# Performance work log

Hardware: AMD Instinct MI355X
Metric: run time of the kernel (lower is better)

Reference implementation:

```python
import jax, jax.numpy as jnp
import numpy as np

NUM_CLASS = 8192
FEAT_DIM = 512
BATCH = 131072


def setup_inputs() -> dict:
    key = jax.random.key(0)
    k1, k2, k3 = jax.random.split(key, 3)
    batch_samples = jax.random.normal(k1, (BATCH, FEAT_DIM), dtype=jnp.float32)
    class_sums = jnp.zeros((NUM_CLASS, FEAT_DIM), dtype=jnp.float32)
    targets = jax.random.randint(k2, (BATCH,), 0, NUM_CLASS, dtype=jnp.int64)
    idx = jax.random.randint(k3, (BATCH,), 0, BATCH, dtype=jnp.int64)
    return {"batch_samples": batch_samples, "class_sums": class_sums,
            "targets": targets, "idx": idx}


def reference(batch_samples, class_sums, targets, idx):
    # Original forward: for each unique label, class_sums[label] += sum of rows
    # of batch_samples with that label. This is exactly a segment-sum
    # (scatter-add by class label) accumulated into class_sums.
    # idx is unused in the forward math (kept for signature fidelity).
    inc = jax.ops.segment_sum(batch_samples, targets, num_segments=NUM_CLASS)
    return class_sums + inc  # updated class_sums buffer [num_class, feat_dim]
```

## Files before the change

### kernel.cpp

```cpp
#include <hip/hip_runtime.h>
#include <hip/hip_bf16.h>


#define FEAT 512
#define FEAT4 128
#define CAP   128

typedef float f4 __attribute__((ext_vector_type(4)));

__device__ __forceinline__ void bucket_one(int c, int row, int* __restrict__ fill,
                                           int* __restrict__ rows_buf,
                                           int* __restrict__ ovf_cnt,
                                           int* __restrict__ ovf) {
    int pos = atomicAdd(&fill[c], 1);
    if (pos < CAP) rows_buf[c * CAP + pos] = row;
    else           ovf[atomicAdd(ovf_cnt, 1)] = row;
}

__global__ void k_scatter(const int4* __restrict__ t4, int* __restrict__ fill,
                          int* __restrict__ rows_buf, int* __restrict__ ovf_cnt,
                          int* __restrict__ ovf, int n4,
                          const int* __restrict__ targets, int batch) {
    int i = blockIdx.x * blockDim.x + threadIdx.x;
    if (i < n4) {
        int4 v = t4[i];
        int r = i * 4;
        bucket_one(v.x, r + 0, fill, rows_buf, ovf_cnt, ovf);
        bucket_one(v.y, r + 1, fill, rows_buf, ovf_cnt, ovf);
        bucket_one(v.z, r + 2, fill, rows_buf, ovf_cnt, ovf);
        bucket_one(v.w, r + 3, fill, rows_buf, ovf_cnt, ovf);
    }
    if (i == 0) {
        for (int k = n4 * 4; k < batch; ++k)
            bucket_one(targets[k], k, fill, rows_buf, ovf_cnt, ovf);
    }
}

__global__ __launch_bounds__(128) void k_sum(const f4* __restrict__ batch,
                                             const f4* __restrict__ csums,
                                             const int* __restrict__ fill,
                                             const int* __restrict__ rows_buf,
                                             f4* __restrict__ out) {
    const int c = blockIdx.x;
    const int t = threadIdx.x;
    const int n = min(fill[c], CAP);

    __shared__ int sidx[CAP];
    if (t < n) sidx[t] = rows_buf[c * CAP + t];
    __syncthreads();

    f4 acc = csums[(size_t)c * FEAT4 + t];

    int j = 0;
    for (; j + 8 <= n; j += 8) {
        f4 v0 = __builtin_nontemporal_load(&batch[(size_t)sidx[j + 0] * FEAT4 + t]);
        f4 v1 = __builtin_nontemporal_load(&batch[(size_t)sidx[j + 1] * FEAT4 + t]);
        f4 v2 = __builtin_nontemporal_load(&batch[(size_t)sidx[j + 2] * FEAT4 + t]);
        f4 v3 = __builtin_nontemporal_load(&batch[(size_t)sidx[j + 3] * FEAT4 + t]);
        f4 v4 = __builtin_nontemporal_load(&batch[(size_t)sidx[j + 4] * FEAT4 + t]);
        f4 v5 = __builtin_nontemporal_load(&batch[(size_t)sidx[j + 5] * FEAT4 + t]);
        f4 v6 = __builtin_nontemporal_load(&batch[(size_t)sidx[j + 6] * FEAT4 + t]);
        f4 v7 = __builtin_nontemporal_load(&batch[(size_t)sidx[j + 7] * FEAT4 + t]);
        acc += ((v0 + v1) + (v2 + v3)) + ((v4 + v5) + (v6 + v7));
    }
    for (; j < n; ++j)
        acc += __builtin_nontemporal_load(&batch[(size_t)sidx[j] * FEAT4 + t]);

    __builtin_nontemporal_store(acc, &out[(size_t)c * FEAT4 + t]);
}

__global__ __launch_bounds__(128) void k_ovf(const f4* __restrict__ batch,
                                             const int* __restrict__ targets,
                                             const int* __restrict__ ovf_cnt,
                                             const int* __restrict__ ovf,
                                             float* __restrict__ out) {
    const int cnt = *ovf_cnt;
    const int t = threadIdx.x;
    for (int e = blockIdx.x; e < cnt; e += gridDim.x) {
        int row = ovf[e];
        int c = targets[row];
        f4 v = batch[(size_t)row * FEAT4 + t];
        float* o = out + (size_t)c * FEAT + t * 4;
        atomicAdd(o + 0, v.x);
        atomicAdd(o + 1, v.y);
        atomicAdd(o + 2, v.z);
        atomicAdd(o + 3, v.w);
    }
}

__global__ void k_copy(const float4* __restrict__ src, float4* __restrict__ dst, int n4) {
    int i = blockIdx.x * blockDim.x + threadIdx.x;
    if (i < n4) dst[i] = src[i];
}

__global__ __launch_bounds__(128) void k_atomic(const float4* __restrict__ batch,
                                                const int* __restrict__ targets,
                                                float* __restrict__ out, int batch_n) {
    const int r = blockIdx.x;
    const int t = threadIdx.x;
    if (r >= batch_n) return;
    float4 v = batch[(size_t)r * FEAT4 + t];
    float* o = out + (size_t)targets[r] * FEAT + t * 4;
    atomicAdd(o + 0, v.x);
    atomicAdd(o + 1, v.y);
    atomicAdd(o + 2, v.z);
    atomicAdd(o + 3, v.w);
}

extern "C" void kernel_launch(void* const* d_in, const int* in_sizes, int n_in,
                              void* d_out, int out_size, void* d_ws, size_t ws_size,
                              hipStream_t stream) {
    const float* batch_samples = (const float*)d_in[0];
    const float* class_sums    = (const float*)d_in[1];
    const int*   targets       = (const int*)d_in[2];

    const int batch     = in_sizes[2];
    const int num_class = out_size / FEAT;
    float* out = (float*)d_out;

    const size_t rows_off = ((size_t)num_class + 64) & ~63ull;
    const size_t ovf_off  = rows_off + (size_t)num_class * CAP;
    const size_t need     = (ovf_off + (size_t)batch) * 4;

    if (ws_size >= need) {
        int* fill     = (int*)d_ws;
        int* ovf_cnt  = fill + num_class;
        int* rows_buf = fill + rows_off;
        int* ovf      = fill + ovf_off;
        const int n4 = batch / 4;

        (void)hipMemsetAsync(fill, 0, ((size_t)num_class + 1) * 4, stream);
        k_scatter<<<(n4 + 255) / 256, 256, 0, stream>>>((const int4*)targets, fill,
                                                        rows_buf, ovf_cnt, ovf,
                                                        n4, targets, batch);
        k_sum<<<num_class, 128, 0, stream>>>((const f4*)batch_samples,
                                             (const f4*)class_sums,
                                             fill, rows_buf, (f4*)out);
        k_ovf<<<256, 128, 0, stream>>>((const f4*)batch_samples, targets,
                                       ovf_cnt, ovf, out);
    } else {
        const int nv4 = out_size / 4;
        k_copy<<<(nv4 + 255) / 256, 256, 0, stream>>>((const float4*)class_sums,
                                                      (float4*)out, nv4);
        k_atomic<<<batch, 128, 0, stream>>>((const float4*)batch_samples,
                                            targets, out, batch);
    }
}
```

Baseline: 377.2 us.

## Replace bucket-and-gather with column-sliced LDS atomic segment-sum kernel

Drops the three-kernel pipeline (bucket rows by class into a workspace, gather-sum per class, overflow atomics) and uses one kernel of 256 blocks. Each block owns one 16-byte feature column slice and half of the class range. It streams all targets, adds matching rows into a 4x4096 shared-memory accumulator with LDS atomics, then writes the result plus class_sums. This removes the memset, the global bucketing atomics and the index workspace. In exchange every block reads the full targets array, batch reads become strided 16-byte accesses across rows, and shared atomics may contend.

```diff
diff --git a/kernel.cpp b/kernel.cpp
--- a/kernel.cpp
+++ b/kernel.cpp
@@ -1,90 +1,76 @@
 #include <hip/hip_runtime.h>
-#include <hip/hip_bf16.h>
 
 
-#define FEAT 512
-#define FEAT4 128
-#define CAP   128
+#define FEAT   512
+#define FEAT4  128
+#define NCLS_MAX 8192
+#define CSPAN  4096
+#define TPB    1024
 
 typedef float f4 __attribute__((ext_vector_type(4)));
 
-__device__ __forceinline__ void bucket_one(int c, int row, int* __restrict__ fill,
-                                           int* __restrict__ rows_buf,
-                                           int* __restrict__ ovf_cnt,
-                                           int* __restrict__ ovf) {
-    int pos = atomicAdd(&fill[c], 1);
-    if (pos < CAP) rows_buf[c * CAP + pos] = row;
-    else           ovf[atomicAdd(ovf_cnt, 1)] = row;
-}
+__global__ __launch_bounds__(TPB) void k_seg(const f4* __restrict__ batch,
+                                             const f4* __restrict__ csums,
+                                             const int4* __restrict__ t4,
+                                             const int* __restrict__ targets,
+                                             f4* __restrict__ out,
+                                             int batch_n, int num_class) {
+    const int bb = blockIdx.x & 127;
+    const int h  = blockIdx.x >> 7;
+    const int s  = ((bb & 15) << 3) | (bb >> 4);
+    const int cbase = h * CSPAN;
+    const int cspan = min(CSPAN, num_class - cbase);
+    if (cspan <= 0) return;
 
-__global__ void k_scatter(const int4* __restrict__ t4, int* __restrict__ fill,
-                          int* __restrict__ rows_buf, int* __restrict__ ovf_cnt,
-                          int* __restrict__ ovf, int n4,
-                          const int* __restrict__ targets, int batch) {
-    int i = blockIdx.x * blockDim.x + threadIdx.x;
-    if (i < n4) {
-        int4 v = t4[i];
-        int r = i * 4;
-        bucket_one(v.x, r + 0, fill, rows_buf, ovf_cnt, ovf);
-        bucket_one(v.y, r + 1, fill, rows_buf, ovf_cnt, ovf);
-        bucket_one(v.z, r + 2, fill, rows_buf, ovf_cnt, ovf);
-        bucket_one(v.w, r + 3, fill, rows_buf, ovf_cnt, ovf);
-    }
-    if (i == 0) {
-        for (int k = n4 * 4; k < batch; ++k)
-            bucket_one(targets[k], k, fill, rows_buf, ovf_cnt, ovf);
-    }
-}
+    __shared__ float acc[4][CSPAN];
 
-__global__ __launch_bounds__(128) void k_sum(const f4* __restrict__ batch,
-                                             const f4* __restrict__ csums,
-                                             const int* __restrict__ fill,
-                                             const int* __restrict__ rows_buf,
-                                             f4* __restrict__ out) {
-    const int c = blockIdx.x;
-    const int t = threadIdx.x;
-    const int n = min(fill[c], CAP);
-
-    __shared__ int sidx[CAP];
-    if (t < n) sidx[t] = rows_buf[c * CAP + t];
+    f4* accv = (f4*)acc;
+    for (int i = threadIdx.x; i < CSPAN; i += TPB) accv[i] = (f4){0.f, 0.f, 0.f, 0.f};
     __syncthreads();
 
-    f4 acc = csums[(size_t)c * FEAT4 + t];
+    const int n4 = batch_n >> 2;
+    for (int i = threadIdx.x; i < n4; i += TPB) {
+        int4 t = t4[i];
+        size_t r = (size_t)i << 2;
+        int c0 = t.x - cbase, c1 = t.y - cbase, c2 = t.z - cbase, c3 = t.w - cbase;
+        if ((unsigned)c0 < (unsigned)cspan) {
+            f4 v = batch[(r + 0) * FEAT4 + s];
+            atomicAdd(&acc[0][c0], v.x); atomicAdd(&acc[1][c0], v.y);
+            atomicAdd(&acc[2][c0], v.z); atomicAdd(&acc[3][c0], v.w);
+        }
+        if ((unsigned)c1 < (unsigned)cspan) {
+            f4 v = batch[(r + 1) * FEAT4 + s];
+            atomicAdd(&acc[0][c1], v.x); atomicAdd(&acc[1][c1], v.y);
+            atomicAdd(&acc[2][c1], v.z); atomicAdd(&acc[3][c1], v.w);
+        }
+        if ((unsigned)c2 < (unsigned)cspan) {
+            f4 v = batch[(r + 2) * FEAT4 + s];
+            atomicAdd(&acc[0][c2], v.x); atomicAdd(&acc[1][c2], v.y);
+            atomicAdd(&acc[2][c2], v.z); atomicAdd(&acc[3][c2], v.w);
+        }
+        if ((unsigned)c3 < (unsigned)cspan) {
+            f4 v = batch[(r + 3) * FEAT4 + s];
+            atomicAdd(&acc[0][c3], v.x); atomicAdd(&acc[1][c3], v.y);
+            atomicAdd(&acc[2][c3], v.z); atomicAdd(&acc[3][c3], v.w);
+        }
+    }
+    if (threadIdx.x < (batch_n & 3)) {
+        int k = (n4 << 2) + threadIdx.x;
+        int c = targets[k] - cbase;
+        if ((unsigned)c < (unsigned)cspan) {
+            f4 v = batch[(size_t)k * FEAT4 + s];
+            atomicAdd(&acc[0][c], v.x); atomicAdd(&acc[1][c], v.y);
+            atomicAdd(&acc[2][c], v.z); atomicAdd(&acc[3][c], v.w);
+        }
+    }
+    __syncthreads();
 
-    int j = 0;
-    for (; j + 8 <= n; j += 8) {
-        f4 v0 = __builtin_nontemporal_load(&batch[(size_t)sidx[j + 0] * FEAT4 + t]);
-        f4 v1 = __builtin_nontemporal_load(&batch[(size_t)sidx[j + 1] * FEAT4 + t]);
-        f4 v2 = __builtin_nontemporal_load(&batch[(size_t)sidx[j + 2] * FEAT4 + t]);
-        f4 v3 = __builtin_nontemporal_load(&batch[(size_t)sidx[j + 3] * FEAT4 + t]);
-        f4 v4 = __builtin_nontemporal_load(&batch[(size_t)sidx[j + 4] * FEAT4 + t]);
-        f4 v5 = __builtin_nontemporal_load(&batch[(size_t)sidx[j + 5] * FEAT4 + t]);
-        f4 v6 = __builtin_nontemporal_load(&batch[(size_t)sidx[j + 6] * FEAT4 + t]);
-        f4 v7 = __builtin_nontemporal_load(&batch[(size_t)sidx[j + 7] * FEAT4 + t]);
-        acc += ((v0 + v1) + (v2 + v3)) + ((v4 + v5) + (v6 + v7));
-    }
-    for (; j < n; ++j)
-        acc += __builtin_nontemporal_load(&batch[(size_t)sidx[j] * FEAT4 + t]);
-
-    __builtin_nontemporal_store(acc, &out[(size_t)c * FEAT4 + t]);
-}
-
-__global__ __launch_bounds__(128) void k_ovf(const f4* __restrict__ batch,
-                                             const int* __restrict__ targets,
-                                             const int* __restrict__ ovf_cnt,
-                                             const int* __restrict__ ovf,
-                                             float* __restrict__ out) {
-    const int cnt = *ovf_cnt;
-    const int t = threadIdx.x;
-    for (int e = blockIdx.x; e < cnt; e += gridDim.x) {
-        int row = ovf[e];
-        int c = targets[row];
-        f4 v = batch[(size_t)row * FEAT4 + t];
-        float* o = out + (size_t)c * FEAT + t * 4;
-        atomicAdd(o + 0, v.x);
-        atomicAdd(o + 1, v.y);
-        atomicAdd(o + 2, v.z);
-        atomicAdd(o + 3, v.w);
+    for (int c = threadIdx.x; c < cspan; c += TPB) {
+        f4 v;
+        v.x = acc[0][c]; v.y = acc[1][c]; v.z = acc[2][c]; v.w = acc[3][c];
+        size_t o = (size_t)(cbase + c) * FEAT4 + s;
+        v += csums[o];
+        out[o] = v;
     }
 }
 
@@ -118,26 +104,15 @@
     const int num_class = out_size / FEAT;
     float* out = (float*)d_out;
 
-    const size_t rows_off = ((size_t)num_class + 64) & ~63ull;
-    const size_t ovf_off  = rows_off + (size_t)num_class * CAP;
-    const size_t need     = (ovf_off + (size_t)batch) * 4;
+    (void)d_ws; (void)ws_size;
 
-    if (ws_size >= need) {
-        int* fill     = (int*)d_ws;
-        int* ovf_cnt  = fill + num_class;
-        int* rows_buf = fill + rows_off;
-        int* ovf      = fill + ovf_off;
-        const int n4 = batch / 4;
+    const int feat = (batch > 0) ? in_sizes[0] / batch : 0;
 
-        (void)hipMemsetAsync(fill, 0, ((size_t)num_class + 1) * 4, stream);
-        k_scatter<<<(n4 + 255) / 256, 256, 0, stream>>>((const int4*)targets, fill,
-                                                        rows_buf, ovf_cnt, ovf,
-                                                        n4, targets, batch);
-        k_sum<<<num_class, 128, 0, stream>>>((const f4*)batch_samples,
-                                             (const f4*)class_sums,
-                                             fill, rows_buf, (f4*)out);
-        k_ovf<<<256, 128, 0, stream>>>((const f4*)batch_samples, targets,
-                                       ovf_cnt, ovf, out);
+    if (num_class >= 1 && num_class <= NCLS_MAX && feat == FEAT) {
+        k_seg<<<256, TPB, 0, stream>>>((const f4*)batch_samples,
+                                       (const f4*)class_sums,
+                                       (const int4*)targets, targets,
+                                       (f4*)out, batch, num_class);
     } else {
         const int nv4 = out_size / 4;
         k_copy<<<(nv4 + 255) / 256, 256, 0, stream>>>((const float4*)class_sums,
```

After: 622.2 us. +64.9%, slower.
